# Performance work log

Measured on AMD Instinct MI355X. Metric: run time of the kernel, lower is better.

The kernel has to match this reference:

```python
import jax, jax.numpy as jnp
import numpy as np
jax.config.update("jax_enable_x64", True)

MS_H = 10
MS_W = 10
EPS = 1e-8


def _window_mean(x, kh, kw):
    # x: [B, H, W]; VALID avg-pool with kernel (kh, kw), stride 1, via integral image
    c = jnp.cumsum(jnp.cumsum(x, axis=1), axis=2)
    c = jnp.pad(c, ((0, 0), (1, 0), (1, 0)))
    H, W = x.shape[1], x.shape[2]
    oh, ow = H - kh + 1, W - kw + 1
    s = (c[:, kh:kh + oh, kw:kw + ow] - c[:, :oh, kw:kw + ow]
         - c[:, kh:kh + oh, :ow] + c[:, :oh, :ow])
    return s / (kh * kw)


def _translate_bilinear(imgs, dy, dx):
    # imgs: [B, H, W]; out[b,i,j] = imgs[b, i - dy[b], j - dx[b]] (bilinear, zero fill)
    B, H, W = imgs.shape
    yq = jnp.arange(H, dtype=imgs.dtype)[None, :, None] - dy[:, None, None]
    xq = jnp.arange(W, dtype=imgs.dtype)[None, None, :] - dx[:, None, None]
    y0 = jnp.floor(yq); x0 = jnp.floor(xq)
    wy = yq - y0;       wx = xq - x0
    y0i = y0.astype(jnp.int32); x0i = x0.astype(jnp.int32)
    b = jnp.arange(B)[:, None, None]
    def samp(yi, xi):
        valid = (yi >= 0) & (yi < H) & (xi >= 0) & (xi < W)
        v = imgs[b, jnp.clip(yi, 0, H - 1), jnp.clip(xi, 0, W - 1)]
        return jnp.where(valid, v, jnp.zeros((), imgs.dtype))
    v00 = samp(y0i, x0i);     v01 = samp(y0i, x0i + 1)
    v10 = samp(y0i + 1, x0i); v11 = samp(y0i + 1, x0i + 1)
    return (v00 * (1 - wy) * (1 - wx) + v01 * (1 - wy) * wx
            + v10 * wy * (1 - wx) + v11 * wy * wx)


def _motion_correct(fr, template):
    # fr: [1, B, H, W, 1] float32; template: [H, W] float32
    B = fr.shape[1]
    H, W = template.shape
    mx, my = H // 2, W // 2
    # --- template normalization ---
    t_zm = template - jnp.mean(template)
    t_var = jnp.sum(jnp.square(t_zm)) + EPS
    target_freq = jnp.fft.fft2(t_zm.astype(jnp.complex128))            # [H, W]
    imgs = fr[0, :, :, :, 0]                                           # [B, H, W]
    imgs_zm = imgs - jnp.mean(imgs, axis=(1, 2), keepdims=True)
    # --- local statistics (avg_pool2d VALID, kernel = template minus shift margins) ---
    kh, kw = H - 2 * MS_W, W - 2 * MS_H
    m1 = _window_mean(imgs, kh, kw)                                    # [B, 2mw+1, 2mh+1]
    m2 = _window_mean(jnp.square(imgs), kh, kw)
    imgs_var = m2 - jnp.square(m1) / (kh * kw) + EPS
    imgs_var = jnp.where(imgs_var < 0, 0.0, imgs_var)
    denominator = jnp.sqrt(t_var * imgs_var)
    # --- FFT cross-correlation (fft3d over batch+spatial, exactly as the TF code) ---
    fr_freq = jnp.fft.fftn(imgs_zm.astype(jnp.complex128), axes=(0, 1, 2))
    img_product = fr_freq * jnp.conj(target_freq)[None]
    cc = jnp.abs(jnp.fft.ifftn(img_product, axes=(0, 1, 2))).astype(jnp.float32)
    rolled = jnp.roll(cc, (B, mx, my), axis=(0, 1, 2))
    nom = rolled[:, mx - MS_W:mx + MS_W + 1, my - MS_H:my + MS_H + 1]
    ncc = nom / denominator
    ncc = jnp.where(jnp.isnan(ncc), 0.0, ncc)                          # [B, 2mw+1, 2mh+1]
    # --- integer peak ---
    flat = ncc.reshape(B, -1)
    am = jnp.argmax(flat, axis=1)
    shx = am // (2 * MS_H + 1)
    shy = am % (2 * MS_H + 1)
    sh_x_n = -(shx - MS_H).astype(jnp.float32)
    sh_y_n = -(shy - MS_W).astype(jnp.float32)
    # --- log-parabolic sub-pixel refinement ---
    l = jnp.log(ncc)
    b = jnp.arange(B)
    lxm1 = l[b, shx - 1, shy]; lxp1 = l[b, shx + 1, shy]
    lym1 = l[b, shx, shy - 1]; lyp1 = l[b, shx, shy + 1]
    lc4 = 4.0 * l[b, shx, shy]
    sh_x_n = sh_x_n - (lxm1 - lxp1) / (2 * lxm1 - lc4 + 2 * lxp1)
    sh_y_n = sh_y_n - (lym1 - lyp1) / (2 * lym1 - lc4 + 2 * lyp1)
    # --- bilinear translate; tfa translations = [sh_y (dx, width), sh_x (dy, height)] ---
    warped = _translate_bilinear(imgs, sh_x_n, sh_y_n)                 # [B, H, W]
    return jnp.transpose(warped, (0, 2, 1)).reshape(B, H * W)


def setup_inputs() -> dict:
    H = W = 512
    B = 32
    k1, k2, k3 = jax.random.split(jax.random.key(0), 3)
    # smooth (low-pass) random template so the NCC peak is smooth/positive around its max
    noise = jax.random.normal(k1, (H, W))
    f = jnp.sqrt(jnp.fft.fftfreq(H)[:, None] ** 2 + jnp.fft.fftfreq(W)[None, :] ** 2)
    lp = (f < 0.05).astype(jnp.complex128)
    template = jnp.real(jnp.fft.ifft2(jnp.fft.fft2(noise) * lp))
    template = (template / template.std()).astype(jnp.float32)
    # frames: template shifted by small random integer offsets + noise
    shifts = jax.random.randint(k2, (B, 2), -5, 6)
    frames = jax.vmap(lambda s: jnp.roll(template, (s[0], s[1]), axis=(0, 1)))(shifts)
    frames = frames + 0.05 * jax.random.normal(k3, (B, H, W), dtype=jnp.float32)
    fr = frames[None, :, :, :, None].astype(jnp.float32)
    return {"fr": fr, "template": template}


def reference(fr, template):
    return _motion_correct(fr, template)
```

## Files before the change

### kernel.cpp

```cpp
#include <hip/hip_runtime.h>
#include <math.h>

#define HH 512
#define WW 512
#define NPIX (HH*WW)
#define NB 32
#define NS 21
#define KWIN 492
#define NKB 512
#define MT28 28
#define PARTSZ (MT28*32*16)

typedef __attribute__((ext_vector_type(8))) short short8;
typedef __attribute__((ext_vector_type(8))) unsigned short ushort8;
typedef __attribute__((ext_vector_type(4))) float floatx4;

__device__ __forceinline__ unsigned short f2bf(float f) {
    unsigned u = __float_as_uint(f);
    unsigned r = (u + 0x7fffu + ((u >> 16) & 1u)) >> 16;
    return (unsigned short)r;
}

__global__ __launch_bounds__(256) void stage1(
    const float* __restrict__ fr, const float* __restrict__ tpl,
    unsigned short* __restrict__ tplv,
    float* __restrict__ I1, float* __restrict__ I2,
    double* __restrict__ sum1, double* __restrict__ sum2)
{
    int blk = blockIdx.x;
    int t   = threadIdx.x;
    if (blk < 512) {
        int id = blk;
        int b  = id >> 4;
        int yg = id & 15;
        int y0, ny;
        if (yg < 8) { y0 = 20 + 30 * yg; ny = 30; }
        else        { y0 = 260 + 29 * (yg - 8); ny = 29; }
        const float* img = fr + (size_t)b * NPIX;
        int xa = t, xb = t + 256;
        float s1a = 0.f, s2a = 0.f, s1b = 0.f, s2b = 0.f;
        for (int y = y0; y < y0 + ny; ++y) {
            float va = img[(size_t)y * WW + xa];
            float vb = img[(size_t)y * WW + xb];
            s1a += va; s2a += va * va;
            s1b += vb; s2b += vb * vb;
        }
        atomicAdd(&I1[b * WW + xa], s1a); atomicAdd(&I2[b * WW + xa], s2a);
        atomicAdd(&I1[b * WW + xb], s1b); atomicAdd(&I2[b * WW + xb], s2b);
    } else if (blk < 520) {
        int gq = blk - 512;
        int y0 = 64 * gq;
        int xa = t, xb = t + 256;
        float s1a = 0.f, s2a = 0.f, s1b = 0.f, s2b = 0.f;
        for (int y = y0; y < y0 + 64; ++y) {
            float va = tpl[(size_t)y * WW + xa];
            float vb = tpl[(size_t)y * WW + xb];
            s1a += va; s2a += va * va;
            s1b += vb; s2b += vb * vb;
        }
        double d1 = (double)s1a + (double)s1b;
        double d2 = (double)s2a + (double)s2b;
        for (int off = 32; off; off >>= 1) {
            d1 += __shfl_down(d1, off);
            d2 += __shfl_down(d2, off);
        }
        __shared__ double r1[4], r2[4];
        int lane = t & 63, wv = t >> 6;
        if (lane == 0) { r1[wv] = d1; r2[wv] = d2; }
        __syncthreads();
        if (t == 0) {
            atomicAdd(&sum1[32], r1[0] + r1[1] + r1[2] + r1[3]);
            atomicAdd(&sum2[32], r2[0] + r2[1] + r2[2] + r2[3]);
        }
    } else {
        int blk2 = blk - 520;
        int dv   = blk2 / 34;
        int prg  = blk2 % 34;
        int prEnd = min(16 * prg + 16, 532);
        int x2 = 2 * t;
        for (int pr = 16 * prg; pr < prEnd; ++pr) {
            int sy = (pr + 502) & 511;
            const float* srow = tpl + (size_t)sy * WW;
            unsigned short* drow = tplv + ((size_t)dv * 532 + pr) * 512;
            int sx0 = (x2     - dv + 522) & 511;
            int sx1 = (x2 + 1 - dv + 522) & 511;
            ushort2 o;
            o.x = f2bf(srow[sx0]);
            o.y = f2bf(srow[sx1]);
            *(ushort2*)(drow + x2) = o;
        }
    }
}

__global__ __launch_bounds__(896) void corr_mfma(
    const float* __restrict__ fr,
    const unsigned short* __restrict__ tplv,
    float* __restrict__ part)
{
    __shared__ unsigned short Bs[16384];

    const int t   = threadIdx.x;
    const int l   = t & 63;
    const int wid = t >> 6;
    const int idx = blockIdx.x;
    const int kb  = ((idx & 7) << 6) | (idx >> 3);
    const int k0  = kb << 9;
    const int kg  = l >> 4;
    const int ln  = l & 15;

    for (int i = t; i < 4096; i += 896) {
        int frame = i >> 7;
        int q     = i & 127;
        float4 v = *(const float4*)(fr + (size_t)frame * NPIX + k0 + 4 * q);
        int k8 = q >> 1, j4 = (q & 1) * 4;
        ushort4 o;
        o.x = f2bf(v.x); o.y = f2bf(v.y); o.z = f2bf(v.z); o.w = f2bf(v.w);
        *(ushort4*)&Bs[(k8 * 32 + frame) * 8 + j4] = o;
    }

    const unsigned short* pA0;
    const unsigned short* pA1;
    {
        int m_g = 32 * wid + ln;
        int du  = (m_g * 1561) >> 15;
        int dv  = m_g - 21 * du;
        if (m_g >= 441) { du = 0; dv = 0; }
        pA0 = tplv + ((size_t)(dv * 532 + 20 - du) * 512 + 8 * kg + k0);
        m_g = 32 * wid + 16 + ln;
        du  = (m_g * 1561) >> 15;
        dv  = m_g - 21 * du;
        if (m_g >= 441) { du = 0; dv = 0; }
        pA1 = tplv + ((size_t)(dv * 532 + 20 - du) * 512 + 8 * kg + k0);
    }

    const unsigned short* lB = Bs + kg * 256 + ln * 8;

    __syncthreads();

    floatx4 acc00 = {}, acc01 = {}, acc10 = {}, acc11 = {};

#pragma unroll
    for (int ks = 0; ks < 16; ++ks) {
        short8 A0 = *(const short8*)pA0;
        short8 A1 = *(const short8*)pA1;
        short8 B0 = *(const short8*)(lB + ks * 1024);
        short8 B1 = *(const short8*)(lB + ks * 1024 + 128);
        acc00 = __builtin_amdgcn_mfma_f32_16x16x32_bf16(A0, B0, acc00, 0, 0, 0);
        acc01 = __builtin_amdgcn_mfma_f32_16x16x32_bf16(A0, B1, acc01, 0, 0, 0);
        acc10 = __builtin_amdgcn_mfma_f32_16x16x32_bf16(A1, B0, acc10, 0, 0, 0);
        acc11 = __builtin_amdgcn_mfma_f32_16x16x32_bf16(A1, B1, acc11, 0, 0, 0);
        pA0 += 32; pA1 += 32;
    }

    {
        size_t base = ((size_t)kb * MT28 + 2 * wid) * 32;
        floatx4* p;
        p = (floatx4*)(part + (base + ln)      * 16 + 4 * kg); *p = acc00;
        p = (floatx4*)(part + (base + 16 + ln) * 16 + 4 * kg); *p = acc01;
        p = (floatx4*)(part + (base + 32 + ln) * 16 + 4 * kg); *p = acc10;
        p = (floatx4*)(part + (base + 48 + ln) * 16 + 4 * kg); *p = acc11;
    }
}

__global__ __launch_bounds__(512) void reduce_stage2(
    const float* __restrict__ part, float* __restrict__ cc,
    const float* __restrict__ fr, const float* __restrict__ I1,
    const float* __restrict__ I2, double* __restrict__ sum1,
    const double* __restrict__ sum2, float* __restrict__ denom)
{
    __shared__ double wr1[NS][8], wr2[NS][8], wrT[8];
    __shared__ float  e1[NS][40], e2[NS][40];
    __shared__ double totals1[NS], totals2[NS];

    int blk = blockIdx.x;
    if (blk < 224) {
        int oct = blk / 28;
        int j   = (blk % 28) * 512 + threadIdx.x;
        const float* p = part + (size_t)(oct * 64) * PARTSZ + j;
        float s = 0.f;
#pragma unroll 8
        for (int i = 0; i < 64; ++i)
            s += p[(size_t)i * PARTSZ];
        int mr    = j & 15;
        int n     = (j >> 4) & 31;
        int mtile = j >> 9;
        int m = mtile * 16 + mr;
        if (m < 441)
            atomicAdd(&cc[(size_t)n * 441 + m], s);
        return;
    }

    int b = blk - 224;
    int x = threadIdx.x;
    const float* img = fr + (size_t)b * NPIX;
    float top[20], bot[20];
#pragma unroll
    for (int y = 0; y < 20; ++y) top[y] = img[(size_t)y * WW + x];
#pragma unroll
    for (int y = 0; y < 20; ++y) bot[y] = img[(size_t)(492 + y) * WW + x];

    float t1 = 0.f, t2 = 0.f, b1 = 0.f, b2 = 0.f;
#pragma unroll
    for (int y = 0; y < 20; ++y) {
        t1 += top[y]; t2 += top[y] * top[y];
        b1 += bot[y]; b2 += bot[y] * bot[y];
    }
    float i1 = I1[b * WW + x], i2 = I2[b * WW + x];
    int lane = x & 63, wv = x >> 6;

    double tot = (double)i1 + (double)t1 + (double)b1;
    for (int off = 32; off; off >>= 1) tot += __shfl_down(tot, off);
    if (lane == 0) wrT[wv] = tot;

    float s1 = i1 + t1, s2 = i2 + t2;
#pragma unroll
    for (int u = 0; u < NS; ++u) {
        if (u) {
            float a = top[u-1], c = bot[u-1];
            s1 += c - a;
            s2 += c * c - a * a;
        }
        double d1 = (double)s1, d2 = (double)s2;
        for (int off = 32; off; off >>= 1) {
            d1 += __shfl_down(d1, off);
            d2 += __shfl_down(d2, off);
        }
        if (lane == 0) { wr1[u][wv] = d1; wr2[u][wv] = d2; }
        if (x < 20)        { e1[u][x]       = s1; e2[u][x]       = s2; }
        else if (x >= 492) { e1[u][x - 472] = s1; e2[u][x - 472] = s2; }
    }
    __syncthreads();
    if (x == 0) {
        double s = 0.0;
        for (int i = 0; i < 8; ++i) s += wrT[i];
        sum1[b] = s;
    }
    if (x < NS) {
        double a = 0.0, c = 0.0;
        for (int i = 0; i < 8; ++i) { a += wr1[x][i]; c += wr2[x][i]; }
        totals1[x] = a; totals2[x] = c;
    }
    __syncthreads();
    if (x < NS * NS) {
        int u = x / NS, v = x - NS * u;
        double S1 = totals1[u], S2 = totals2[u];
        for (int j = 0; j < v; ++j)  { S1 -= (double)e1[u][j];      S2 -= (double)e2[u][j]; }
        for (int j = v; j < 20; ++j) { S1 -= (double)e1[u][20 + j]; S2 -= (double)e2[u][20 + j]; }
        const double inv = 1.0 / ((double)KWIN * (double)KWIN);
        double m1 = S1 * inv, m2 = S2 * inv;
        double var = m2 - (m1 * m1) * inv + 1e-8;
        if (var < 0.0) var = 0.0;
        double tv = sum2[32] - sum1[32] * sum1[32] * (1.0 / (double)NPIX) + 1e-8;
        denom[(size_t)b * NS * NS + x] = (float)sqrt(tv * var);
    }
}

__global__ __launch_bounds__(64) void argmax_kernel(
    const float* __restrict__ cc, const float* __restrict__ denom,
    const double* __restrict__ sum1, float* __restrict__ shifts)
{
    int b = blockIdx.x;
    const float* C = cc    + (size_t)b * NS * NS;
    const float* D = denom + (size_t)b * NS * NS;
    float corr = (float)(sum1[b] * sum1[32] * (1.0 / (double)NPIX));
    int l = threadIdx.x;
    float best = -1e30f; int bidx = NS * NS;
    for (int i = l; i < NS * NS; i += 64) {
        float v = fabsf(C[i] - corr) / D[i];
        if (v != v) v = 0.f;
        if (v > best) { best = v; bidx = i; }
    }
    for (int off = 32; off; off >>= 1) {
        float ov = __shfl_down(best, off);
        int   oi = __shfl_down(bidx, off);
        if (ov > best || (ov == best && oi < bidx)) { best = ov; bidx = oi; }
    }
    if (l == 0) {
        int shx = bidx / NS, shy = bidx % NS;
        auto nccAt = [&](int i, int j) -> float {
            i = (i < 0) ? i + NS : i; i = (i > NS - 1) ? NS - 1 : i;
            j = (j < 0) ? j + NS : j; j = (j > NS - 1) ? NS - 1 : j;
            float v = fabsf(C[i * NS + j] - corr) / D[i * NS + j];
            if (v != v) v = 0.f;
            return v;
        };
        float lc  = logf(nccAt(shx, shy));
        float lxm = logf(nccAt(shx - 1, shy));
        float lxp = logf(nccAt(shx + 1, shy));
        float lym = logf(nccAt(shx, shy - 1));
        float lyp = logf(nccAt(shx, shy + 1));
        float shxn = -(float)(shx - 10) - (lxm - lxp) / (2.f * lxm - 4.f * lc + 2.f * lxp);
        float shyn = -(float)(shy - 10) - (lym - lyp) / (2.f * lym - 4.f * lc + 2.f * lyp);
        shifts[b]      = shxn;
        shifts[32 + b] = shyn;
    }
}

__device__ __forceinline__ float samp(const float* __restrict__ img, int y, int x) {
    bool valid = (y >= 0) & (y < HH) & (x >= 0) & (x < WW);
    int yc = min(max(y, 0), HH - 1), xc = min(max(x, 0), WW - 1);
    float v = img[(size_t)yc * WW + xc];
    return valid ? v : 0.f;
}

__global__ __launch_bounds__(256) void warp_kernel(
    const float* __restrict__ fr, const float* __restrict__ shifts,
    float* __restrict__ out)
{
    int b  = blockIdx.z;
    int h0 = blockIdx.y * 32;
    int w0 = blockIdx.x * 32;
    float dy = shifts[b], dx = shifts[32 + b];
    const float* img = fr + (size_t)b * NPIX;
    __shared__ float tile[32][33];
    int tx = threadIdx.x & 31;
    int tz = threadIdx.x >> 5;
#pragma unroll
    for (int s = 0; s < 4; ++s) {
        int h = h0 + tz + 8 * s;
        int w = w0 + tx;
        float yq = (float)h - dy;
        float xq = (float)w - dx;
        float y0f = floorf(yq), x0f = floorf(xq);
        float wy = yq - y0f, wx = xq - x0f;
        int y0 = (int)y0f, x0 = (int)x0f;
        float v00 = samp(img, y0,     x0);
        float v01 = samp(img, y0,     x0 + 1);
        float v10 = samp(img, y0 + 1, x0);
        float v11 = samp(img, y0 + 1, x0 + 1);
        float val = v00 * (1.f - wy) * (1.f - wx) + v01 * (1.f - wy) * wx
                  + v10 * wy * (1.f - wx)         + v11 * wy * wx;
        tile[tz + 8 * s][tx] = val;
    }
    __syncthreads();
#pragma unroll
    for (int s = 0; s < 4; ++s) {
        int hh = tx;
        int ww = tz + 8 * s;
        out[(size_t)b * NPIX + (size_t)(w0 + ww) * HH + (h0 + hh)] = tile[hh][ww];
    }
}

extern "C" void kernel_launch(void* const* d_in, const int* in_sizes, int n_in,
                              void* d_out, int out_size, void* d_ws, size_t ws_size,
                              hipStream_t stream) {
    const float* fr  = (const float*)d_in[0];
    const float* tpl = (const float*)d_in[1];
    float* out = (float*)d_out;
    char* ws = (char*)d_ws;

    double* sum1    = (double*)(ws + 0);
    double* sum2    = (double*)(ws + 512);
    float*  cc      = (float*) (ws + 4096);
    float*  I1      = (float*) (ws + 61440);
    float*  I2      = (float*) (ws + 126976);
    float*  shifts  = (float*) (ws + 196608);
    float*  denom   = (float*) (ws + 200704);
    unsigned short* tplv = (unsigned short*)(ws + 262144);
    float*  part    = (float*) (ws + 16777216);

    hipMemsetAsync(ws, 0, 192512, stream);

    stage1       <<<1234, 256, 0, stream>>>(fr, tpl, tplv, I1, I2, sum1, sum2);
    corr_mfma    <<<512, 896, 0, stream>>>(fr, tplv, part);
    reduce_stage2<<<256, 512, 0, stream>>>(part, cc, fr, I1, I2, sum1, sum2, denom);
    argmax_kernel<<<32, 64, 0, stream>>>(cc, denom, sum1, shifts);
    warp_kernel  <<<dim3(16, 16, 32), 256, 0, stream>>>(fr, shifts, out);
}
```

Baseline: 167.1 us.

## Fuse all stages into one cooperative persistent kernel with grid syncs

```diff
diff --git a/kernel.cpp b/kernel.cpp
--- a/kernel.cpp
+++ b/kernel.cpp
@@ -1,5 +1,8 @@
 #include <hip/hip_runtime.h>
+#include <hip/hip_cooperative_groups.h>
 #include <math.h>
+
+namespace cg = cooperative_groups;
 
 #define HH 512
 #define WW 512
@@ -7,12 +10,10 @@
 #define NB 32
 #define NS 21
 #define KWIN 492
-#define NKB 512
 #define MT28 28
 #define PARTSZ (MT28*32*16)
 
 typedef __attribute__((ext_vector_type(8))) short short8;
-typedef __attribute__((ext_vector_type(8))) unsigned short ushort8;
 typedef __attribute__((ext_vector_type(4))) float floatx4;
 
 __device__ __forceinline__ unsigned short f2bf(float f) {
@@ -21,323 +22,346 @@
     return (unsigned short)r;
 }
 
-__global__ __launch_bounds__(256) void stage1(
+__global__ __launch_bounds__(512) void motion_all(
     const float* __restrict__ fr, const float* __restrict__ tpl,
-    unsigned short* __restrict__ tplv,
-    float* __restrict__ I1, float* __restrict__ I2,
-    double* __restrict__ sum1, double* __restrict__ sum2)
+    unsigned short* __restrict__ tplv, float* __restrict__ part,
+    float* __restrict__ cc8, float* __restrict__ I1p, float* __restrict__ I2p,
+    double* __restrict__ tplS1p, double* __restrict__ tplS2p,
+    double* __restrict__ sum1, float* __restrict__ denom,
+    float* __restrict__ shifts, float* __restrict__ out)
 {
-    int blk = blockIdx.x;
-    int t   = threadIdx.x;
-    if (blk < 512) {
-        int id = blk;
-        int b  = id >> 4;
-        int yg = id & 15;
-        int y0, ny;
-        if (yg < 8) { y0 = 20 + 30 * yg; ny = 30; }
-        else        { y0 = 260 + 29 * (yg - 8); ny = 29; }
+    cg::grid_group grid = cg::this_grid();
+
+    __shared__ unsigned short Bs[16384];
+    __shared__ float tile2[2][32][33];
+    __shared__ double wr1[NS][8], wr2[NS][8], wrT[8];
+    __shared__ float  e1[NS][40], e2[NS][40];
+    __shared__ double totals1[NS], totals2[NS];
+    __shared__ double jb1[8], jb2[8];
+    __shared__ double tS1s, tS2s;
+
+    const int blk = blockIdx.x;
+    const int t   = threadIdx.x;
+
+    {
+        int b = blk >> 3, oct = blk & 7;
         const float* img = fr + (size_t)b * NPIX;
-        int xa = t, xb = t + 256;
-        float s1a = 0.f, s2a = 0.f, s1b = 0.f, s2b = 0.f;
-        for (int y = y0; y < y0 + ny; ++y) {
-            float va = img[(size_t)y * WW + xa];
-            float vb = img[(size_t)y * WW + xb];
-            s1a += va; s2a += va * va;
-            s1b += vb; s2b += vb * vb;
-        }
-        atomicAdd(&I1[b * WW + xa], s1a); atomicAdd(&I2[b * WW + xa], s2a);
-        atomicAdd(&I1[b * WW + xb], s1b); atomicAdd(&I2[b * WW + xb], s2b);
-    } else if (blk < 520) {
-        int gq = blk - 512;
-        int y0 = 64 * gq;
-        int xa = t, xb = t + 256;
-        float s1a = 0.f, s2a = 0.f, s1b = 0.f, s2b = 0.f;
-        for (int y = y0; y < y0 + 64; ++y) {
-            float va = tpl[(size_t)y * WW + xa];
-            float vb = tpl[(size_t)y * WW + xb];
-            s1a += va; s2a += va * va;
-            s1b += vb; s2b += vb * vb;
-        }
-        double d1 = (double)s1a + (double)s1b;
-        double d2 = (double)s2a + (double)s2b;
+        int x = t;
+        float s1 = 0.f, s2 = 0.f;
+        int y0 = 20 + 59 * oct;
+        for (int y = y0; y < y0 + 59; ++y) {
+            float v = img[(size_t)y * WW + x];
+            s1 += v; s2 += v * v;
+        }
+        I1p[(size_t)blk * 512 + x] = s1;
+        I2p[(size_t)blk * 512 + x] = s2;
+    }
+    {
+        int rbeg = 44 * blk;
+        int rend = min(rbeg + 44, NS * 532);
+        int rp = t >> 8;
+        int xi = (t & 255) * 2;
+        for (int r2 = rbeg; r2 < rend; r2 += 2) {
+            int r = r2 + rp;
+            if (r < rend) {
+                int dv = r / 532;
+                int pr = r - 532 * dv;
+                int sy = (pr + 502) & 511;
+                const float* srow = tpl + (size_t)sy * WW;
+                unsigned short* drow = tplv + (size_t)r * 512;
+                int sx0 = (xi     - dv + 522) & 511;
+                int sx1 = (xi + 1 - dv + 522) & 511;
+                ushort2 o;
+                o.x = f2bf(srow[sx0]);
+                o.y = f2bf(srow[sx1]);
+                *(ushort2*)(drow + xi) = o;
+            }
+        }
+    }
+    if ((blk & 3) == 3) {
+        int tj = blk >> 2;
+        const float* trow = tpl + (size_t)tj * 8 * WW;
+        float s1 = 0.f, s2 = 0.f;
+        int x = t;
+        for (int y = 0; y < 8; ++y) {
+            float v = trow[(size_t)y * WW + x];
+            s1 += v; s2 += v * v;
+        }
+        double d1 = (double)s1, d2 = (double)s2;
         for (int off = 32; off; off >>= 1) {
             d1 += __shfl_down(d1, off);
             d2 += __shfl_down(d2, off);
         }
-        __shared__ double r1[4], r2[4];
         int lane = t & 63, wv = t >> 6;
-        if (lane == 0) { r1[wv] = d1; r2[wv] = d2; }
+        if (lane == 0) { jb1[wv] = d1; jb2[wv] = d2; }
         __syncthreads();
         if (t == 0) {
-            atomicAdd(&sum1[32], r1[0] + r1[1] + r1[2] + r1[3]);
-            atomicAdd(&sum2[32], r2[0] + r2[1] + r2[2] + r2[3]);
-        }
-    } else {
-        int blk2 = blk - 520;
-        int dv   = blk2 / 34;
-        int prg  = blk2 % 34;
-        int prEnd = min(16 * prg + 16, 532);
-        int x2 = 2 * t;
-        for (int pr = 16 * prg; pr < prEnd; ++pr) {
-            int sy = (pr + 502) & 511;
-            const float* srow = tpl + (size_t)sy * WW;
-            unsigned short* drow = tplv + ((size_t)dv * 532 + pr) * 512;
-            int sx0 = (x2     - dv + 522) & 511;
-            int sx1 = (x2 + 1 - dv + 522) & 511;
-            ushort2 o;
-            o.x = f2bf(srow[sx0]);
-            o.y = f2bf(srow[sx1]);
-            *(ushort2*)(drow + x2) = o;
-        }
-    }
-}
-
-__global__ __launch_bounds__(896) void corr_mfma(
-    const float* __restrict__ fr,
-    const unsigned short* __restrict__ tplv,
-    float* __restrict__ part)
-{
-    __shared__ unsigned short Bs[16384];
-
-    const int t   = threadIdx.x;
-    const int l   = t & 63;
-    const int wid = t >> 6;
-    const int idx = blockIdx.x;
-    const int kb  = ((idx & 7) << 6) | (idx >> 3);
-    const int k0  = kb << 9;
-    const int kg  = l >> 4;
-    const int ln  = l & 15;
-
-    for (int i = t; i < 4096; i += 896) {
-        int frame = i >> 7;
-        int q     = i & 127;
-        float4 v = *(const float4*)(fr + (size_t)frame * NPIX + k0 + 4 * q);
-        int k8 = q >> 1, j4 = (q & 1) * 4;
-        ushort4 o;
-        o.x = f2bf(v.x); o.y = f2bf(v.y); o.z = f2bf(v.z); o.w = f2bf(v.w);
-        *(ushort4*)&Bs[(k8 * 32 + frame) * 8 + j4] = o;
-    }
-
-    const unsigned short* pA0;
-    const unsigned short* pA1;
+            double a = 0.0, c = 0.0;
+            for (int i = 0; i < 8; ++i) { a += jb1[i]; c += jb2[i]; }
+            tplS1p[tj] = a; tplS2p[tj] = c;
+        }
+    }
+
+    grid.sync();
+
     {
-        int m_g = 32 * wid + ln;
-        int du  = (m_g * 1561) >> 15;
-        int dv  = m_g - 21 * du;
-        if (m_g >= 441) { du = 0; dv = 0; }
-        pA0 = tplv + ((size_t)(dv * 532 + 20 - du) * 512 + 8 * kg + k0);
-        m_g = 32 * wid + 16 + ln;
-        du  = (m_g * 1561) >> 15;
-        dv  = m_g - 21 * du;
-        if (m_g >= 441) { du = 0; dv = 0; }
-        pA1 = tplv + ((size_t)(dv * 532 + 20 - du) * 512 + 8 * kg + k0);
-    }
-
-    const unsigned short* lB = Bs + kg * 256 + ln * 8;
-
-    __syncthreads();
-
-    floatx4 acc00 = {}, acc01 = {}, acc10 = {}, acc11 = {};
-
-#pragma unroll
-    for (int ks = 0; ks < 16; ++ks) {
-        short8 A0 = *(const short8*)pA0;
-        short8 A1 = *(const short8*)pA1;
-        short8 B0 = *(const short8*)(lB + ks * 1024);
-        short8 B1 = *(const short8*)(lB + ks * 1024 + 128);
-        acc00 = __builtin_amdgcn_mfma_f32_16x16x32_bf16(A0, B0, acc00, 0, 0, 0);
-        acc01 = __builtin_amdgcn_mfma_f32_16x16x32_bf16(A0, B1, acc01, 0, 0, 0);
-        acc10 = __builtin_amdgcn_mfma_f32_16x16x32_bf16(A1, B0, acc10, 0, 0, 0);
-        acc11 = __builtin_amdgcn_mfma_f32_16x16x32_bf16(A1, B1, acc11, 0, 0, 0);
-        pA0 += 32; pA1 += 32;
-    }
-
-    {
-        size_t base = ((size_t)kb * MT28 + 2 * wid) * 32;
-        floatx4* p;
-        p = (floatx4*)(part + (base + ln)      * 16 + 4 * kg); *p = acc00;
-        p = (floatx4*)(part + (base + 16 + ln) * 16 + 4 * kg); *p = acc01;
-        p = (floatx4*)(part + (base + 32 + ln) * 16 + 4 * kg); *p = acc10;
-        p = (floatx4*)(part + (base + 48 + ln) * 16 + 4 * kg); *p = acc11;
-    }
-}
-
-__global__ __launch_bounds__(512) void reduce_stage2(
-    const float* __restrict__ part, float* __restrict__ cc,
-    const float* __restrict__ fr, const float* __restrict__ I1,
-    const float* __restrict__ I2, double* __restrict__ sum1,
-    const double* __restrict__ sum2, float* __restrict__ denom)
-{
-    __shared__ double wr1[NS][8], wr2[NS][8], wrT[8];
-    __shared__ float  e1[NS][40], e2[NS][40];
-    __shared__ double totals1[NS], totals2[NS];
-
-    int blk = blockIdx.x;
+        const int l  = t & 63;
+        const int w  = t >> 6;
+        const int kg = l >> 4;
+        const int ln = l & 15;
+        const int kbA = ((blk & 7) << 6) | (blk >> 3);
+#pragma unroll 1
+        for (int c = 0; c < 2; ++c) {
+            const int kb = kbA + 32 * c;
+            const int k0 = kb << 9;
+            if (c) __syncthreads();
+            for (int i = t; i < 4096; i += 512) {
+                int frame = i >> 7, q = i & 127;
+                float4 v = *(const float4*)(fr + (size_t)frame * NPIX + k0 + 4 * q);
+                int k8 = q >> 1, j4 = (q & 1) * 4;
+                ushort4 o;
+                o.x = f2bf(v.x); o.y = f2bf(v.y); o.z = f2bf(v.z); o.w = f2bf(v.w);
+                *(ushort4*)&Bs[(k8 * 32 + frame) * 8 + j4] = o;
+            }
+            __syncthreads();
+            if (w < 7) {
+                const unsigned short *q0, *q1, *q2, *q3;
+                {
+                    int m_g, du, dv;
+                    m_g = 16 * (4 * w + 0) + ln; du = (m_g * 1561) >> 15; dv = m_g - 21 * du;
+                    if (m_g >= 441) { du = 0; dv = 0; }
+                    q0 = tplv + ((size_t)(dv * 532 + 20 - du) * 512 + 8 * kg + k0);
+                    m_g = 16 * (4 * w + 1) + ln; du = (m_g * 1561) >> 15; dv = m_g - 21 * du;
+                    if (m_g >= 441) { du = 0; dv = 0; }
+                    q1 = tplv + ((size_t)(dv * 532 + 20 - du) * 512 + 8 * kg + k0);
+                    m_g = 16 * (4 * w + 2) + ln; du = (m_g * 1561) >> 15; dv = m_g - 21 * du;
+                    if (m_g >= 441) { du = 0; dv = 0; }
+                    q2 = tplv + ((size_t)(dv * 532 + 20 - du) * 512 + 8 * kg + k0);
+                    m_g = 16 * (4 * w + 3) + ln; du = (m_g * 1561) >> 15; dv = m_g - 21 * du;
+                    if (m_g >= 441) { du = 0; dv = 0; }
+                    q3 = tplv + ((size_t)(dv * 532 + 20 - du) * 512 + 8 * kg + k0);
+                }
+                const unsigned short* lB = Bs + kg * 256 + ln * 8;
+                floatx4 a00 = {}, a01 = {}, a10 = {}, a11 = {};
+                floatx4 a20 = {}, a21 = {}, a30 = {}, a31 = {};
+#pragma unroll
+                for (int ks = 0; ks < 16; ++ks) {
+                    short8 A0 = *(const short8*)q0;
+                    short8 A1 = *(const short8*)q1;
+                    short8 A2 = *(const short8*)q2;
+                    short8 A3 = *(const short8*)q3;
+                    short8 B0 = *(const short8*)(lB + ks * 1024);
+                    short8 B1 = *(const short8*)(lB + ks * 1024 + 128);
+                    a00 = __builtin_amdgcn_mfma_f32_16x16x32_bf16(A0, B0, a00, 0, 0, 0);
+                    a01 = __builtin_amdgcn_mfma_f32_16x16x32_bf16(A0, B1, a01, 0, 0, 0);
+                    a10 = __builtin_amdgcn_mfma_f32_16x16x32_bf16(A1, B0, a10, 0, 0, 0);
+                    a11 = __builtin_amdgcn_mfma_f32_16x16x32_bf16(A1, B1, a11, 0, 0, 0);
+                    a20 = __builtin_amdgcn_mfma_f32_16x16x32_bf16(A2, B0, a20, 0, 0, 0);
+                    a21 = __builtin_amdgcn_mfma_f32_16x16x32_bf16(A2, B1, a21, 0, 0, 0);
+                    a30 = __builtin_amdgcn_mfma_f32_16x16x32_bf16(A3, B0, a30, 0, 0, 0);
+                    a31 = __builtin_amdgcn_mfma_f32_16x16x32_bf16(A3, B1, a31, 0, 0, 0);
+                    q0 += 32; q1 += 32; q2 += 32; q3 += 32;
+                }
+                size_t base = ((size_t)kb * MT28 + 4 * w) * 32;
+                floatx4* p;
+                p = (floatx4*)(part + (base +       ln) * 16 + 4 * kg); *p = a00;
+                p = (floatx4*)(part + (base +  16 + ln) * 16 + 4 * kg); *p = a01;
+                p = (floatx4*)(part + (base +  32 + ln) * 16 + 4 * kg); *p = a10;
+                p = (floatx4*)(part + (base +  48 + ln) * 16 + 4 * kg); *p = a11;
+                p = (floatx4*)(part + (base +  64 + ln) * 16 + 4 * kg); *p = a20;
+                p = (floatx4*)(part + (base +  80 + ln) * 16 + 4 * kg); *p = a21;
+                p = (floatx4*)(part + (base +  96 + ln) * 16 + 4 * kg); *p = a30;
+                p = (floatx4*)(part + (base + 112 + ln) * 16 + 4 * kg); *p = a31;
+            }
+        }
+    }
+
+    grid.sync();
+
     if (blk < 224) {
         int oct = blk / 28;
-        int j   = (blk % 28) * 512 + threadIdx.x;
+        int j   = (blk % 28) * 512 + t;
         const float* p = part + (size_t)(oct * 64) * PARTSZ + j;
         float s = 0.f;
 #pragma unroll 8
         for (int i = 0; i < 64; ++i)
             s += p[(size_t)i * PARTSZ];
-        int mr    = j & 15;
-        int n     = (j >> 4) & 31;
-        int mtile = j >> 9;
-        int m = mtile * 16 + mr;
-        if (m < 441)
-            atomicAdd(&cc[(size_t)n * 441 + m], s);
-        return;
-    }
-
-    int b = blk - 224;
-    int x = threadIdx.x;
-    const float* img = fr + (size_t)b * NPIX;
-    float top[20], bot[20];
-#pragma unroll
-    for (int y = 0; y < 20; ++y) top[y] = img[(size_t)y * WW + x];
-#pragma unroll
-    for (int y = 0; y < 20; ++y) bot[y] = img[(size_t)(492 + y) * WW + x];
-
-    float t1 = 0.f, t2 = 0.f, b1 = 0.f, b2 = 0.f;
-#pragma unroll
-    for (int y = 0; y < 20; ++y) {
-        t1 += top[y]; t2 += top[y] * top[y];
-        b1 += bot[y]; b2 += bot[y] * bot[y];
-    }
-    float i1 = I1[b * WW + x], i2 = I2[b * WW + x];
-    int lane = x & 63, wv = x >> 6;
-
-    double tot = (double)i1 + (double)t1 + (double)b1;
-    for (int off = 32; off; off >>= 1) tot += __shfl_down(tot, off);
-    if (lane == 0) wrT[wv] = tot;
-
-    float s1 = i1 + t1, s2 = i2 + t2;
-#pragma unroll
-    for (int u = 0; u < NS; ++u) {
-        if (u) {
-            float a = top[u-1], c = bot[u-1];
-            s1 += c - a;
-            s2 += c * c - a * a;
-        }
-        double d1 = (double)s1, d2 = (double)s2;
+        cc8[(size_t)oct * PARTSZ + j] = s;
+    } else if (blk < 256) {
+        int b = blk - 224;
+        int x = t;
+        const float* img = fr + (size_t)b * NPIX;
+        float top[20], bot[20];
+#pragma unroll
+        for (int y = 0; y < 20; ++y) top[y] = img[(size_t)y * WW + x];
+#pragma unroll
+        for (int y = 0; y < 20; ++y) bot[y] = img[(size_t)(492 + y) * WW + x];
+
+        float t1 = 0.f, t2 = 0.f, b1 = 0.f, b2 = 0.f;
+#pragma unroll
+        for (int y = 0; y < 20; ++y) {
+            t1 += top[y]; t2 += top[y] * top[y];
+            b1 += bot[y]; b2 += bot[y] * bot[y];
+        }
+        float i1 = 0.f, i2 = 0.f;
+#pragma unroll
+        for (int o = 0; o < 8; ++o) {
+            i1 += I1p[((size_t)(b * 8 + o)) * 512 + x];
+            i2 += I2p[((size_t)(b * 8 + o)) * 512 + x];
+        }
+        int lane = x & 63, wv = x >> 6;
+
+        if (x < 64) {
+            double d1 = tplS1p[x], d2 = tplS2p[x];
+            for (int off = 32; off; off >>= 1) {
+                d1 += __shfl_down(d1, off);
+                d2 += __shfl_down(d2, off);
+            }
+            if (x == 0) {
+                tS1s = d1; tS2s = d2;
+                if (blk == 224) { sum1[32] = d1; }
+            }
+        }
+
+        double tot = (double)i1 + (double)t1 + (double)b1;
+        for (int off = 32; off; off >>= 1) tot += __shfl_down(tot, off);
+        if (lane == 0) wrT[wv] = tot;
+
+        float s1 = i1 + t1, s2 = i2 + t2;
+#pragma unroll
+        for (int u = 0; u < NS; ++u) {
+            if (u) {
+                float a = top[u-1], c = bot[u-1];
+                s1 += c - a;
+                s2 += c * c - a * a;
+            }
+            double d1 = (double)s1, d2 = (double)s2;
+            for (int off = 32; off; off >>= 1) {
+                d1 += __shfl_down(d1, off);
+                d2 += __shfl_down(d2, off);
+            }
+            if (lane == 0) { wr1[u][wv] = d1; wr2[u][wv] = d2; }
+            if (x < 20)        { e1[u][x]       = s1; e2[u][x]       = s2; }
+            else if (x >= 492) { e1[u][x - 472] = s1; e2[u][x - 472] = s2; }
+        }
+        __syncthreads();
+        if (x == 0) {
+            double s = 0.0;
+            for (int i = 0; i < 8; ++i) s += wrT[i];
+            sum1[b] = s;
+        }
+        if (x < NS) {
+            double a = 0.0, c = 0.0;
+            for (int i = 0; i < 8; ++i) { a += wr1[x][i]; c += wr2[x][i]; }
+            totals1[x] = a; totals2[x] = c;
+        }
+        __syncthreads();
+        if (x < NS * NS) {
+            int u = x / NS, v = x - NS * u;
+            double S1 = totals1[u], S2 = totals2[u];
+            for (int j = 0; j < v; ++j)  { S1 -= (double)e1[u][j];      S2 -= (double)e2[u][j]; }
+            for (int j = v; j < 20; ++j) { S1 -= (double)e1[u][20 + j]; S2 -= (double)e2[u][20 + j]; }
+            const double inv = 1.0 / ((double)KWIN * (double)KWIN);
+            double m1 = S1 * inv, m2 = S2 * inv;
+            double var = m2 - (m1 * m1) * inv + 1e-8;
+            if (var < 0.0) var = 0.0;
+            double tv = tS2s - tS1s * tS1s * (1.0 / (double)NPIX) + 1e-8;
+            denom[(size_t)b * NS * NS + x] = (float)sqrt(tv * var);
+        }
+    }
+
+    grid.sync();
+
+    if (blk < NB && t < 64) {
+        int b = blk;
+        const float* D = denom + (size_t)b * NS * NS;
+        float corr = (float)(sum1[b] * sum1[32] * (1.0 / (double)NPIX));
+        auto ccAt = [&](int m) -> float {
+            int jj = ((m >> 4) * 512) + b * 16 + (m & 15);
+            float s = 0.f;
+#pragma unroll
+            for (int o = 0; o < 8; ++o) s += cc8[(size_t)o * PARTSZ + jj];
+            return s;
+        };
+        int l = t;
+        float best = -1e30f; int bidx = NS * NS;
+        for (int i = l; i < NS * NS; i += 64) {
+            float v = fabsf(ccAt(i) - corr) / D[i];
+            if (v != v) v = 0.f;
+            if (v > best) { best = v; bidx = i; }
+        }
         for (int off = 32; off; off >>= 1) {
-            d1 += __shfl_down(d1, off);
-            d2 += __shfl_down(d2, off);
-        }
-        if (lane == 0) { wr1[u][wv] = d1; wr2[u][wv] = d2; }
-        if (x < 20)        { e1[u][x]       = s1; e2[u][x]       = s2; }
-        else if (x >= 492) { e1[u][x - 472] = s1; e2[u][x - 472] = s2; }
-    }
-    __syncthreads();
-    if (x == 0) {
-        double s = 0.0;
-        for (int i = 0; i < 8; ++i) s += wrT[i];
-        sum1[b] = s;
-    }
-    if (x < NS) {
-        double a = 0.0, c = 0.0;
-        for (int i = 0; i < 8; ++i) { a += wr1[x][i]; c += wr2[x][i]; }
-        totals1[x] = a; totals2[x] = c;
-    }
-    __syncthreads();
-    if (x < NS * NS) {
-        int u = x / NS, v = x - NS * u;
-        double S1 = totals1[u], S2 = totals2[u];
-        for (int j = 0; j < v; ++j)  { S1 -= (double)e1[u][j];      S2 -= (double)e2[u][j]; }
-        for (int j = v; j < 20; ++j) { S1 -= (double)e1[u][20 + j]; S2 -= (double)e2[u][20 + j]; }
-        const double inv = 1.0 / ((double)KWIN * (double)KWIN);
-        double m1 = S1 * inv, m2 = S2 * inv;
-        double var = m2 - (m1 * m1) * inv + 1e-8;
-        if (var < 0.0) var = 0.0;
-        double tv = sum2[32] - sum1[32] * sum1[32] * (1.0 / (double)NPIX) + 1e-8;
-        denom[(size_t)b * NS * NS + x] = (float)sqrt(tv * var);
-    }
-}
-
-__global__ __launch_bounds__(64) void argmax_kernel(
-    const float* __restrict__ cc, const float* __restrict__ denom,
-    const double* __restrict__ sum1, float* __restrict__ shifts)
-{
-    int b = blockIdx.x;
-    const float* C = cc    + (size_t)b * NS * NS;
-    const float* D = denom + (size_t)b * NS * NS;
-    float corr = (float)(sum1[b] * sum1[32] * (1.0 / (double)NPIX));
-    int l = threadIdx.x;
-    float best = -1e30f; int bidx = NS * NS;
-    for (int i = l; i < NS * NS; i += 64) {
-        float v = fabsf(C[i] - corr) / D[i];
-        if (v != v) v = 0.f;
-        if (v > best) { best = v; bidx = i; }
-    }
-    for (int off = 32; off; off >>= 1) {
-        float ov = __shfl_down(best, off);
-        int   oi = __shfl_down(bidx, off);
-        if (ov > best || (ov == best && oi < bidx)) { best = ov; bidx = oi; }
-    }
-    if (l == 0) {
-        int shx = bidx / NS, shy = bidx % NS;
-        auto nccAt = [&](int i, int j) -> float {
-            i = (i < 0) ? i + NS : i; i = (i > NS - 1) ? NS - 1 : i;
-            j = (j < 0) ? j + NS : j; j = (j > NS - 1) ? NS - 1 : j;
-            float v = fabsf(C[i * NS + j] - corr) / D[i * NS + j];
-            if (v != v) v = 0.f;
-            return v;
-        };
-        float lc  = logf(nccAt(shx, shy));
-        float lxm = logf(nccAt(shx - 1, shy));
-        float lxp = logf(nccAt(shx + 1, shy));
-        float lym = logf(nccAt(shx, shy - 1));
-        float lyp = logf(nccAt(shx, shy + 1));
-        float shxn = -(float)(shx - 10) - (lxm - lxp) / (2.f * lxm - 4.f * lc + 2.f * lxp);
-        float shyn = -(float)(shy - 10) - (lym - lyp) / (2.f * lym - 4.f * lc + 2.f * lyp);
-        shifts[b]      = shxn;
-        shifts[32 + b] = shyn;
-    }
-}
-
-__device__ __forceinline__ float samp(const float* __restrict__ img, int y, int x) {
-    bool valid = (y >= 0) & (y < HH) & (x >= 0) & (x < WW);
-    int yc = min(max(y, 0), HH - 1), xc = min(max(x, 0), WW - 1);
-    float v = img[(size_t)yc * WW + xc];
-    return valid ? v : 0.f;
-}
-
-__global__ __launch_bounds__(256) void warp_kernel(
-    const float* __restrict__ fr, const float* __restrict__ shifts,
-    float* __restrict__ out)
-{
-    int b  = blockIdx.z;
-    int h0 = blockIdx.y * 32;
-    int w0 = blockIdx.x * 32;
-    float dy = shifts[b], dx = shifts[32 + b];
-    const float* img = fr + (size_t)b * NPIX;
-    __shared__ float tile[32][33];
-    int tx = threadIdx.x & 31;
-    int tz = threadIdx.x >> 5;
-#pragma unroll
-    for (int s = 0; s < 4; ++s) {
-        int h = h0 + tz + 8 * s;
-        int w = w0 + tx;
-        float yq = (float)h - dy;
-        float xq = (float)w - dx;
-        float y0f = floorf(yq), x0f = floorf(xq);
-        float wy = yq - y0f, wx = xq - x0f;
-        int y0 = (int)y0f, x0 = (int)x0f;
-        float v00 = samp(img, y0,     x0);
-        float v01 = samp(img, y0,     x0 + 1);
-        float v10 = samp(img, y0 + 1, x0);
-        float v11 = samp(img, y0 + 1, x0 + 1);
-        float val = v00 * (1.f - wy) * (1.f - wx) + v01 * (1.f - wy) * wx
-                  + v10 * wy * (1.f - wx)         + v11 * wy * wx;
-        tile[tz + 8 * s][tx] = val;
-    }
-    __syncthreads();
-#pragma unroll
-    for (int s = 0; s < 4; ++s) {
-        int hh = tx;
-        int ww = tz + 8 * s;
-        out[(size_t)b * NPIX + (size_t)(w0 + ww) * HH + (h0 + hh)] = tile[hh][ww];
+            float ov = __shfl_down(best, off);
+            int   oi = __shfl_down(bidx, off);
+            if (ov > best || (ov == best && oi < bidx)) { best = ov; bidx = oi; }
+        }
+        if (l == 0) {
+            int shx = bidx / NS, shy = bidx % NS;
+            auto nccAt = [&](int i, int j) -> float {
+                i = (i < 0) ? i + NS : i; i = (i > NS - 1) ? NS - 1 : i;
+                j = (j < 0) ? j + NS : j; j = (j > NS - 1) ? NS - 1 : j;
+                float v = fabsf(ccAt(i * NS + j) - corr) / D[i * NS + j];
+                if (v != v) v = 0.f;
+                return v;
+            };
+            float lc  = logf(nccAt(shx, shy));
+            float lxm = logf(nccAt(shx - 1, shy));
+            float lxp = logf(nccAt(shx + 1, shy));
+            float lym = logf(nccAt(shx, shy - 1));
+            float lyp = logf(nccAt(shx, shy + 1));
+            float shxn = -(float)(shx - 10) - (lxm - lxp) / (2.f * lxm - 4.f * lc + 2.f * lxp);
+            float shyn = -(float)(shy - 10) - (lym - lyp) / (2.f * lym - 4.f * lc + 2.f * lyp);
+            shifts[b]      = shxn;
+            shifts[32 + b] = shyn;
+        }
+    }
+
+    grid.sync();
+
+    {
+        int g   = t >> 8;
+        int tid = t & 255;
+        int tx  = tid & 31;
+        int tz  = tid >> 5;
+#pragma unroll 1
+        for (int it = 0; it < 16; ++it) {
+            int J = (blk * 2 + g) * 16 + it;
+            int b    = J >> 8;
+            int tile = J & 255;
+            int h0 = (tile >> 4) * 32;
+            int w0 = (tile & 15) * 32;
+            float dy = shifts[b], dx = shifts[32 + b];
+            const float* img = fr + (size_t)b * NPIX;
+#pragma unroll
+            for (int s = 0; s < 4; ++s) {
+                int h = h0 + tz + 8 * s;
+                int w = w0 + tx;
+                float yq = (float)h - dy;
+                float xq = (float)w - dx;
+                float y0f = floorf(yq), x0f = floorf(xq);
+                float wy = yq - y0f, wx = xq - x0f;
+                int y0 = (int)y0f, x0 = (int)x0f;
+                bool vy0 = (y0 >= 0) & (y0 < HH), vy1 = (y0+1 >= 0) & (y0+1 < HH);
+                bool vx0 = (x0 >= 0) & (x0 < WW), vx1 = (x0+1 >= 0) & (x0+1 < WW);
+                int y0c = min(max(y0, 0), HH-1), y1c = min(max(y0+1, 0), HH-1);
+                int x0c = min(max(x0, 0), WW-1), x1c = min(max(x0+1, 0), WW-1);
+                float v00 = (vy0 & vx0) ? img[(size_t)y0c * WW + x0c] : 0.f;
+                float v01 = (vy0 & vx1) ? img[(size_t)y0c * WW + x1c] : 0.f;
+                float v10 = (vy1 & vx0) ? img[(size_t)y1c * WW + x0c] : 0.f;
+                float v11 = (vy1 & vx1) ? img[(size_t)y1c * WW + x1c] : 0.f;
+                float val = v00 * (1.f - wy) * (1.f - wx) + v01 * (1.f - wy) * wx
+                          + v10 * wy * (1.f - wx)         + v11 * wy * wx;
+                tile2[g][tz + 8 * s][tx] = val;
+            }
+            __syncthreads();
+#pragma unroll
+            for (int s = 0; s < 4; ++s) {
+                int hh = tx;
+                int ww = tz + 8 * s;
+                out[(size_t)b * NPIX + (size_t)(w0 + ww) * HH + (h0 + hh)] = tile2[g][hh][ww];
+            }
+            __syncthreads();
+        }
     }
 }
 
@@ -349,21 +373,22 @@
     float* out = (float*)d_out;
     char* ws = (char*)d_ws;
 
-    double* sum1    = (double*)(ws + 0);
-    double* sum2    = (double*)(ws + 512);
-    float*  cc      = (float*) (ws + 4096);
-    float*  I1      = (float*) (ws + 61440);
-    float*  I2      = (float*) (ws + 126976);
-    float*  shifts  = (float*) (ws + 196608);
-    float*  denom   = (float*) (ws + 200704);
-    unsigned short* tplv = (unsigned short*)(ws + 262144);
-    float*  part    = (float*) (ws + 16777216);
-
-    hipMemsetAsync(ws, 0, 192512, stream);
-
-    stage1       <<<1234, 256, 0, stream>>>(fr, tpl, tplv, I1, I2, sum1, sum2);
-    corr_mfma    <<<512, 896, 0, stream>>>(fr, tplv, part);
-    reduce_stage2<<<256, 512, 0, stream>>>(part, cc, fr, I1, I2, sum1, sum2, denom);
-    argmax_kernel<<<32, 64, 0, stream>>>(cc, denom, sum1, shifts);
-    warp_kernel  <<<dim3(16, 16, 32), 256, 0, stream>>>(fr, shifts, out);
+    unsigned short* tplv = (unsigned short*)(ws + 0);
+    float*  part   = (float*) (ws + 16777216);
+    float*  cc8    = (float*) (ws + 50331648);
+    float*  I1p    = (float*) (ws + 51380224);
+    float*  I2p    = (float*) (ws + 52428800);
+    double* tplS1p = (double*)(ws + 53477376);
+    double* tplS2p = (double*)(ws + 53481472);
+    double* sum1   = (double*)(ws + 53485568);
+    float*  denom  = (float*) (ws + 53501952);
+    float*  shifts = (float*) (ws + 53608448);
+
+    void* kargs[] = {
+        (void*)&fr, (void*)&tpl, (void*)&tplv, (void*)&part, (void*)&cc8,
+        (void*)&I1p, (void*)&I2p, (void*)&tplS1p, (void*)&tplS2p,
+        (void*)&sum1, (void*)&denom, (void*)&shifts, (void*)&out
+    };
+    hipLaunchCooperativeKernel((void*)motion_all, dim3(256), dim3(512),
+                               kargs, 0, stream);
 }
```

New measurement: 308.2 us. +84.5%, slower.
